# Kernel optimization log

Hardware: AMD Instinct MI355X
Metric: run time of the kernel (lower is better)

Reference implementation:

```python
import jax, jax.numpy as jnp
import numpy as np
from jax import lax

jax.config.update("jax_enable_x64", True)

B = 32768          # batch size
NCS = 96           # number of charging stations
NB = 124           # num_buses
S_BASE = 1000.0
MAX_CS = 22.17
MIN_CS = -22.17
MAX_EV_CH = 22.0
MAX_EV_DIS = -22.0
EV_CAP = 70.0
EV_MIN_CAP = 15.0
ITERS = 100
TOL = 1e-06
DT = 15.0 / 60.0   # timescale (hours)


def setup_inputs() -> dict:
    ks = jax.random.split(jax.random.key(0), 12)
    action = jax.random.uniform(ks[0], (B, NCS), dtype=jnp.float32, minval=-1.0, maxval=1.0)
    prices = jax.random.uniform(ks[1], (B, 1), dtype=jnp.float32, minval=0.05, maxval=0.5)
    active = jax.random.uniform(ks[2], (B, NB - 1), dtype=jnp.float32, minval=0.0, maxval=50.0)
    reactive = jax.random.uniform(ks[3], (B, NB - 1), dtype=jnp.float32, minval=0.0, maxval=20.0)
    cap = jax.random.uniform(ks[4], (B, NCS), dtype=jnp.float32, minval=0.0, maxval=EV_CAP)
    cap = cap * (jax.random.uniform(ks[5], (B, NCS)) > 0.2).astype(jnp.float32)
    tleft = jax.random.randint(ks[6], (B, NCS), 1, 10).astype(jnp.float32)
    bus = jax.random.randint(ks[7], (B, NCS), 0, NB - 1).astype(jnp.float32)
    ev = jnp.stack([cap, tleft, bus], axis=-1).reshape(B, 3 * NCS)  # interleaved triples
    state = jnp.concatenate(
        [jnp.zeros((B, 3), jnp.float32), prices, active, reactive, ev], axis=1
    )  # (B, 4 + 2*(NB-1) + 3*NCS) == (B, 538)
    K_re = (0.005 * jax.random.normal(ks[8], (NB - 1, NB - 1))).astype(jnp.float32)
    K_im = (0.005 * jax.random.normal(ks[9], (NB - 1, NB - 1))).astype(jnp.float32)
    L_re = jnp.ones((NB - 1,), jnp.float32)
    L_im = jnp.zeros((NB - 1,), jnp.float32)
    return {"action": action, "state": state, "K_re": K_re, "K_im": K_im, "L_re": L_re, "L_im": L_im}


def _forward(action, state, K_re, K_im, L_re, L_im):
    b, ncs = action.shape
    nb1 = NB - 1
    es = 4 + 2 * nb1  # start of EV state block
    prices = state[:, 3:4]                                    # (B,1), broadcast over stations
    cap = state[:, es:es + 3 * ncs:3]                         # current capacity
    tleft = state[:, es + 1:es + 1 + 3 * ncs:3]               # time left
    bus = state[:, es + 2:es + 2 + 3 * ncs:3].astype(jnp.int32)  # connected bus index
    conn = (cap > 0).astype(action.dtype)
    max_ch = jnp.minimum(MAX_EV_CH, conn * (EV_CAP - cap) / DT)
    max_dis = jnp.maximum(MAX_EV_DIS, conn * (EV_MIN_CAP - cap) / DT)
    pos = jnp.where(action >= 0, 1.0, 0.0).astype(action.dtype)
    power = action * MAX_CS * pos - action * MIN_CS * (1.0 - pos)
    power = jnp.maximum(jnp.minimum(power, max_ch), max_dis)
    costs = (prices * power * DT).sum(axis=1)
    new_cap = jnp.ceil((cap + power * DT) * 100.0) / 100.0
    dep = (tleft == 1).astype(action.dtype)
    user_sat = (-10.0 * dep * (new_cap - EV_CAP) ** 2).sum(axis=1)
    # scatter-add EV power per bus (duplicate indices accumulate, like torch scatter_add)
    ev_bus = jnp.zeros((b, nb1), power.dtype).at[jnp.arange(b)[:, None], bus].add(power)
    ap = state[:, 4:4 + nb1]
    rp = state[:, 4 + nb1:4 + 2 * nb1]
    S = ((ap + ev_bus) / S_BASE + 1j * (rp / S_BASE)).astype(jnp.complex128)  # (B, NB-1)
    K = (K_re + 1j * K_im).astype(jnp.complex128)
    W = (L_re + 1j * L_im).astype(jnp.complex128)
    v_init = jnp.ones((b, nb1), jnp.complex128)

    def run(v0):
        # Z-bus fixed point: v_k = K @ conj(S / v0)^T + W   (batched as bi)
        vk = jnp.einsum('ij,bj->bi', K, jnp.conj(S / v0)) + W
        tol = jnp.max(jnp.abs(jnp.abs(vk) - jnp.abs(v0)))
        return vk, tol

    def body(carry, _):
        v0, done = carry
        def step(v):
            vk, tol = run(v)
            return vk, tol < TOL
        def skip(v):
            return v, jnp.array(True)
        v_next, conv = lax.cond(done, skip, step, v0)
        return (v_next, done | conv), None

    (v_fin, _), _ = lax.scan(body, (v_init, jnp.array(False)), None, length=ITERS)
    vmag = jnp.abs(v_fin)
    voltage_loss = jnp.minimum(0.0, 0.05 - jnp.abs(1.0 - vmag)).sum(axis=1)
    loss = 1000.0 * voltage_loss + costs + user_sat
    return loss.astype(jnp.float32)


def reference(action, state, K_re, K_im, L_re, L_im):
    return _forward(action, state, K_re, K_im, L_re, L_im)
```

## Files before the change

### kernel.cpp

```cpp
#include <hip/hip_runtime.h>

#define NB1   123
#define NCSd  96
#define SW    538
#define TPB   256
#define BT    16
#define STPB  128


__global__ __launch_bounds__(256) void k_norm(const float* __restrict__ Kre,
                                              const float* __restrict__ Kim,
                                              const float* __restrict__ Lre,
                                              const float* __restrict__ Lim,
                                              float* __restrict__ ws) {
    __shared__ float part[4];
    const int tid = threadIdx.x;
    const int w = tid >> 6, l = tid & 63;
    const int wid = blockIdx.x * 4 + w;
    const int j1 = wid, j2 = wid + 64;
    const bool has2 = j2 < NB1;

    const float* kr1 = Kre + j1 * NB1; const float* ki1 = Kim + j1 * NB1;
    float a0 = kr1[l], b0 = ki1[l];
    float a1 = 0.f, b1 = 0.f;
    if (l < NB1 - 64) { a1 = kr1[l + 64]; b1 = ki1[l + 64]; }
    float c0 = 0.f, d0 = 0.f, c1 = 0.f, d1 = 0.f;
    if (has2) {
        const float* kr2 = Kre + j2 * NB1; const float* ki2 = Kim + j2 * NB1;
        c0 = kr2[l]; d0 = ki2[l];
        if (l < NB1 - 64) { c1 = kr2[l + 64]; d1 = ki2[l + 64]; }
    }
    float s1 = fmaf(a0, a0, b0 * b0) + fmaf(a1, a1, b1 * b1);
    float s2 = fmaf(c0, c0, d0 * d0) + fmaf(c1, c1, d1 * d1);
    #pragma unroll
    for (int off = 32; off; off >>= 1) {
        s1 += __shfl_xor(s1, off);
        s2 += __shfl_xor(s2, off);
    }
    float m2 = has2 ? fmaxf(s1, s2) : s1;
    if (l == 0) part[w] = m2;
    __syncthreads();
    if (tid == 0)
        ws[1 + blockIdx.x] = fmaxf(fmaxf(part[0], part[1]), fmaxf(part[2], part[3]));

    if (blockIdx.x == 0 && w == 0) {
        float dr = Lre[l] - 1.f, di = Lim[l];
        float d2 = fmaf(dr, dr, di * di);
        if (l + 64 < NB1) {
            float dr2 = Lre[l + 64] - 1.f, di2 = Lim[l + 64];
            d2 = fmaxf(d2, fmaf(dr2, dr2, di2 * di2));
        }
        #pragma unroll
        for (int off = 32; off; off >>= 1) d2 = fmaxf(d2, __shfl_xor(d2, off));
        if (l == 0) ws[0] = d2;
    }
}

__global__ __launch_bounds__(TPB, 7) void k_fast(const float* __restrict__ action,
                                                 const float* __restrict__ state,
                                                 const float* __restrict__ Kre,
                                                 const float* __restrict__ Kim,
                                                 const float* __restrict__ Lre,
                                                 const float* __restrict__ Lim,
                                                 const float* __restrict__ ws,
                                                 float* __restrict__ out) {
    __shared__ __align__(16) float st[4][1088];
    __shared__ float ev[4][256];

    const int tid = threadIdx.x;
    const int w = tid >> 6, l = tid & 63;
    const long g = (long)blockIdx.x * 4 + w;

    const float4* G4 = (const float4*)(state + g * (2 * SW));
    float4 v0 = G4[l];
    float4 v1 = G4[l + 64];
    float4 v2 = G4[l + 128];
    float4 v3 = G4[l + 192];
    float4 v4 = make_float4(0.f, 0.f, 0.f, 0.f);
    const bool t4 = l < 269 - 256;
    if (t4) v4 = G4[l + 256];

    float r2p = (l < 16) ? ws[1 + l] : 0.f;
    float dw2 = ws[0];

    ev[w][l] = 0.f; ev[w][l + 64] = 0.f;
    ev[w][l + 128] = 0.f; ev[w][l + 192] = 0.f;

    float4* st4 = (float4*)st[w];
    st4[l] = v0; st4[l + 64] = v1; st4[l + 128] = v2; st4[l + 192] = v3;
    if (t4) st4[l + 256] = v4;

    const int e = l >> 5, li = l & 31;
    const long b = 2 * g + e;
    const float* srow = st[w] + e * SW;
    const float* actp = action + b * NCSd;
    float* evp = ev[w] + e * 128;
    const float pr = srow[3];

    float cost = 0.f, usat = 0.f;
    #pragma unroll
    for (int s = 0; s < 3; ++s) {
        int i = li + 32 * s;
        float cap = srow[250 + 3 * i];
        float tl  = srow[251 + 3 * i];
        int   bus = (int)srow[252 + 3 * i];
        float a   = actp[i];
        float conn = cap > 0.f ? 1.f : 0.f;
        float mch = fminf(22.0f,  conn * (70.0f - cap) * 4.0f);
        float mds = fmaxf(-22.0f, conn * (15.0f - cap) * 4.0f);
        float p = fmaxf(fminf(22.17f * a, mch), mds);
        cost = fmaf(pr * p, 0.25f, cost);
        float nc = ceilf((cap + p * 0.25f) * 100.0f) * 0.01f;
        if (tl == 1.0f) { float d = nc - 70.0f; usat = fmaf(-10.0f * d, d, usat); }
        atomicAdd(&evp[bus], p);
    }

    float s2 = 0.f;
    #pragma unroll
    for (int s = 0; s < 4; ++s) {
        int k = li + 32 * s;
        if (k < NB1) {
            float apv = srow[4 + k] + evp[k];
            float rpv = srow[127 + k];
            s2 = fmaf(apv, apv, fmaf(rpv, rpv, s2));
        }
    }
    #pragma unroll
    for (int off = 16; off; off >>= 1) {
        s2   += __shfl_xor(s2, off);
        cost += __shfl_xor(cost, off);
        usat += __shfl_xor(usat, off);
    }

    #pragma unroll
    for (int off = 8; off; off >>= 1) r2p = fmaxf(r2p, __shfl_xor(r2p, off));
    float R  = sqrtf(__shfl(r2p, 0));
    float dW = sqrtf(dw2);
    float t = 0.0495f - dW;
    float q2max = -1.0f;
    if (t > 0.f && t < 1.0f - dW) {
        float xm = (t * (1.0f - dW - t) - 1e-7f) / 1.001f;
        if (xm > 0.f && R > 0.f) {
            float sm = xm / R * 1000.0f;
            q2max = sm * sm;
        }
    }
    bool safe = s2 <= q2max;

    float vs0 = 0.f, vs1 = 0.f;
    unsigned long long bad = __ballot(!safe);
    if (bad & 0x100000001ull) {
        const int j1 = l, j2 = 64 + l;
        const bool has2 = j2 < NB1;
        float* cw = st[w];
        #pragma unroll 1
        for (int fe = 0; fe < 2; ++fe) {
            if (!((bad >> (fe * 32)) & 1ull)) continue;
            const float* frow = st[w] + fe * SW;
            float* fev = ev[w] + fe * 128;
            float S1r = (frow[4 + j1] + fev[j1]) * 0.001f;
            float S1i = frow[127 + j1] * 0.001f;
            float S2r = has2 ? (frow[4 + j2] + fev[j2]) * 0.001f : 0.f;
            float S2i = has2 ? frow[127 + j2] * 0.001f : 0.f;
            float W1r = Lre[j1], W1i = Lim[j1];
            float W2r = has2 ? Lre[j2] : 1.f;
            float W2i = has2 ? Lim[j2] : 0.f;
            float v1r = 1.f, v1i = 0.f, v2r = 1.f, v2i = 0.f;
            for (int it = 0; it < 32; ++it) {
                float d1 = v1r * v1r + v1i * v1i, i1 = 1.0f / d1;
                cw[j1]       = (S1r * v1r + S1i * v1i) * i1;
                cw[128 + j1] = (S1r * v1i - S1i * v1r) * i1;
                if (has2) {
                    float d2 = v2r * v2r + v2i * v2i, i2 = 1.0f / d2;
                    cw[j2]       = (S2r * v2r + S2i * v2i) * i2;
                    cw[128 + j2] = (S2r * v2i - S2i * v2r) * i2;
                }
                asm volatile("s_waitcnt lgkmcnt(0)" ::: "memory");
                float a1r = W1r, a1i = W1i, a2r = W2r, a2i = W2i;
                for (int k = 0; k < NB1; ++k) {
                    float cr = cw[k], ci = cw[128 + k];
                    float kr1 = Kre[j1 * NB1 + k], ki1 = Kim[j1 * NB1 + k];
                    a1r = fmaf(kr1, cr, fmaf(-ki1, ci, a1r));
                    a1i = fmaf(kr1, ci, fmaf( ki1, cr, a1i));
                    if (has2) {
                        float kr2 = Kre[j2 * NB1 + k], ki2 = Kim[j2 * NB1 + k];
                        a2r = fmaf(kr2, cr, fmaf(-ki2, ci, a2r));
                        a2i = fmaf(kr2, ci, fmaf( ki2, cr, a2i));
                    }
                }
                v1r = a1r; v1i = a1i; v2r = a2r; v2i = a2i;
                asm volatile("s_waitcnt lgkmcnt(0)" ::: "memory");
            }
            float vm1 = sqrtf(v1r * v1r + v1i * v1i);
            float vl = fminf(0.f, 0.05f - fabsf(1.0f - vm1));
            if (has2) {
                float vm2 = sqrtf(v2r * v2r + v2i * v2i);
                vl += fminf(0.f, 0.05f - fabsf(1.0f - vm2));
            }
            #pragma unroll
            for (int off = 32; off; off >>= 1) vl += __shfl_xor(vl, off);
            if (fe == 0) vs0 = vl; else vs1 = vl;
        }
    }

    if (li == 0) out[b] = cost + usat + 1000.0f * (e == 0 ? vs0 : vs1);
}

__global__ __launch_bounds__(STPB) void k_main(
    const float* __restrict__ action, const float* __restrict__ state,
    const float* __restrict__ Kre, const float* __restrict__ Kim,
    const float* __restrict__ Lre, const float* __restrict__ Lim,
    float* __restrict__ out)
{
    __shared__ float ev[BT][STPB];
    __shared__ float costs_s[BT];
    __shared__ float usat_s[BT];
    __shared__ __align__(16) float2 cmat[STPB][BT + 2];
    __shared__ float vls[STPB][BT + 1];
    __shared__ float red[2];
    const int tid = threadIdx.x;
    const int e0  = blockIdx.x * BT;
    for (int x = tid; x < BT * STPB; x += STPB) ((float*)ev)[x] = 0.f;
    if (tid < BT) { costs_s[tid] = 0.f; usat_s[tid] = 0.f; }
    __syncthreads();
    for (int task = tid; task < BT * NCSd; task += STPB) {
        int e = task / NCSd, i = task - e * NCSd;
        long b = (long)(e0 + e);
        const float* srow = state + b * SW;
        float cap = srow[250 + 3 * i], tleft = srow[251 + 3 * i];
        int bus = (int)srow[252 + 3 * i];
        float a = action[b * NCSd + i];
        float conn = cap > 0.f ? 1.f : 0.f;
        float mch = fminf(22.0f, conn * (70.0f - cap) * 4.0f);
        float mds = fmaxf(-22.0f, conn * (15.0f - cap) * 4.0f);
        float power = fmaxf(fminf(22.17f * a, mch), mds);
        atomicAdd(&costs_s[e], srow[3] * power * 0.25f);
        float nc = ceilf((cap + power * 0.25f) * 100.0f) * 0.01f;
        if (tleft == 1.0f) { float d = nc - 70.0f; atomicAdd(&usat_s[e], -10.0f * d * d); }
        atomicAdd(&ev[e][bus], power);
    }
    __syncthreads();
    const int j = tid;
    const bool jok = j < NB1;
    float Wre = jok ? Lre[j] : 1.0f, Wim = jok ? Lim[j] : 0.0f;
    float Sre[BT], Sim[BT], vr[BT], vi[BT];
    #pragma unroll
    for (int e = 0; e < BT; ++e) {
        long b = (long)(e0 + e);
        float ap = jok ? state[b * SW + 4 + j] : 0.f;
        float rp = jok ? state[b * SW + 127 + j] : 0.f;
        Sre[e] = (ap + ev[e][j]) * 0.001f; Sim[e] = rp * 0.001f;
        vr[e] = 1.f; vi[e] = 0.f;
    }
    for (int it = 0; it < 100; ++it) {
        #pragma unroll
        for (int e = 0; e < BT; ++e) {
            float d = vr[e]*vr[e] + vi[e]*vi[e];
            float inv = 1.0f / d;
            cmat[j][e] = make_float2((Sre[e]*vr[e] + Sim[e]*vi[e]) * inv,
                                     (Sre[e]*vi[e] - Sim[e]*vr[e]) * inv);
        }
        __syncthreads();
        float ar[BT], ai[BT];
        #pragma unroll
        for (int e = 0; e < BT; ++e) { ar[e] = Wre; ai[e] = Wim; }
        for (int k = 0; k < NB1; ++k) {
            float kr = jok ? Kre[j*NB1+k] : 0.f;
            float ki = jok ? Kim[j*NB1+k] : 0.f;
            const float4* crow = (const float4*)(&cmat[k][0]);
            #pragma unroll
            for (int eh = 0; eh < BT / 2; ++eh) {
                float4 c2 = crow[eh];
                ar[2*eh]   = fmaf(kr, c2.x, fmaf(-ki, c2.y, ar[2*eh]));
                ai[2*eh]   = fmaf(kr, c2.y, fmaf( ki, c2.x, ai[2*eh]));
                ar[2*eh+1] = fmaf(kr, c2.z, fmaf(-ki, c2.w, ar[2*eh+1]));
                ai[2*eh+1] = fmaf(kr, c2.w, fmaf( ki, c2.z, ai[2*eh+1]));
            }
        }
        float md = 0.f;
        #pragma unroll
        for (int e = 0; e < BT; ++e) {
            float vmn = sqrtf(ar[e]*ar[e] + ai[e]*ai[e]);
            float vmo = sqrtf(vr[e]*vr[e] + vi[e]*vi[e]);
            md = fmaxf(md, fabsf(vmn - vmo));
            vr[e] = ar[e]; vi[e] = ai[e];
        }
        #pragma unroll
        for (int off = 32; off > 0; off >>= 1) md = fmaxf(md, __shfl_xor(md, off));
        if ((tid & 63) == 0) red[tid >> 6] = md;
        __syncthreads();
        if (fmaxf(red[0], red[1]) < 1e-6f) break;
    }
    #pragma unroll
    for (int e = 0; e < BT; ++e) {
        float vm = sqrtf(vr[e]*vr[e] + vi[e]*vi[e]);
        vls[j][e] = jok ? fminf(0.f, 0.05f - fabsf(1.0f - vm)) : 0.f;
    }
    __syncthreads();
    if (tid < BT) {
        float s = 0.f;
        for (int k = 0; k < NB1; ++k) s += vls[k][tid];
        out[e0 + tid] = 1000.0f * s + costs_s[tid] + usat_s[tid];
    }
}

extern "C" void kernel_launch(void* const* d_in, const int* in_sizes, int n_in,
                              void* d_out, int out_size, void* d_ws, size_t ws_size,
                              hipStream_t stream) {
    const float* action = (const float*)d_in[0];
    const float* state  = (const float*)d_in[1];
    const float* Kre    = (const float*)d_in[2];
    const float* Kim    = (const float*)d_in[3];
    const float* Lre    = (const float*)d_in[4];
    const float* Lim    = (const float*)d_in[5];
    float* out = (float*)d_out;
    const int B = out_size;

    if (ws_size >= 17 * sizeof(float)) {
        float* ws = (float*)d_ws;
        hipLaunchKernelGGL(k_norm, dim3(16), dim3(256), 0, stream, Kre, Kim, Lre, Lim, ws);
        hipLaunchKernelGGL(k_fast, dim3(B / 8), dim3(TPB), 0, stream,
                           action, state, Kre, Kim, Lre, Lim, ws, out);
    } else {
        hipLaunchKernelGGL(k_main, dim3((B + BT - 1) / BT), dim3(STPB), 0, stream,
                           action, state, Kre, Kim, Lre, Lim, out);
    }
}
```

Before: 36.20 us.

## Make k_fast persistent with register prefetch of next state rows

Replaces the one-shot grid of B/8 blocks with a fixed grid of 1536 blocks. Each wave now loops over up to three row pairs and loads the next pair's state rows into registers while it computes on the current pair. The per-wave setup (reading the norm workspace and computing the safety bound) runs once per wave instead of once per pair. The aim is to hide global-load latency and amortise setup. In exchange, register pressure rises (launch bounds drop from 7 to 6 blocks per SM) and fewer waves are in flight to cover latency.

```diff
diff --git a/kernel.cpp b/kernel.cpp
--- a/kernel.cpp
+++ b/kernel.cpp
@@ -6,6 +6,8 @@
 #define TPB   256
 #define BT    16
 #define STPB  128
+#define NBLK  1536
+#define NWAVE (NBLK * 4)
 
 
 __global__ __launch_bounds__(256) void k_norm(const float* __restrict__ Kre,
@@ -56,82 +58,28 @@
     }
 }
 
-__global__ __launch_bounds__(TPB, 7) void k_fast(const float* __restrict__ action,
+__global__ __launch_bounds__(TPB, 6) void k_fast(const float* __restrict__ action,
                                                  const float* __restrict__ state,
                                                  const float* __restrict__ Kre,
                                                  const float* __restrict__ Kim,
                                                  const float* __restrict__ Lre,
                                                  const float* __restrict__ Lim,
                                                  const float* __restrict__ ws,
-                                                 float* __restrict__ out) {
+                                                 float* __restrict__ out,
+                                                 int P) {
     __shared__ __align__(16) float st[4][1088];
     __shared__ float ev[4][256];
 
     const int tid = threadIdx.x;
     const int w = tid >> 6, l = tid & 63;
-    const long g = (long)blockIdx.x * 4 + w;
-
-    const float4* G4 = (const float4*)(state + g * (2 * SW));
-    float4 v0 = G4[l];
-    float4 v1 = G4[l + 64];
-    float4 v2 = G4[l + 128];
-    float4 v3 = G4[l + 192];
-    float4 v4 = make_float4(0.f, 0.f, 0.f, 0.f);
+    const int e = l >> 5, li = l & 31;
     const bool t4 = l < 269 - 256;
-    if (t4) v4 = G4[l + 256];
+    float4* st4 = (float4*)st[w];
+    float* evp = ev[w] + e * 128;
+    const float* srow = st[w] + e * SW;
 
     float r2p = (l < 16) ? ws[1 + l] : 0.f;
     float dw2 = ws[0];
-
-    ev[w][l] = 0.f; ev[w][l + 64] = 0.f;
-    ev[w][l + 128] = 0.f; ev[w][l + 192] = 0.f;
-
-    float4* st4 = (float4*)st[w];
-    st4[l] = v0; st4[l + 64] = v1; st4[l + 128] = v2; st4[l + 192] = v3;
-    if (t4) st4[l + 256] = v4;
-
-    const int e = l >> 5, li = l & 31;
-    const long b = 2 * g + e;
-    const float* srow = st[w] + e * SW;
-    const float* actp = action + b * NCSd;
-    float* evp = ev[w] + e * 128;
-    const float pr = srow[3];
-
-    float cost = 0.f, usat = 0.f;
-    #pragma unroll
-    for (int s = 0; s < 3; ++s) {
-        int i = li + 32 * s;
-        float cap = srow[250 + 3 * i];
-        float tl  = srow[251 + 3 * i];
-        int   bus = (int)srow[252 + 3 * i];
-        float a   = actp[i];
-        float conn = cap > 0.f ? 1.f : 0.f;
-        float mch = fminf(22.0f,  conn * (70.0f - cap) * 4.0f);
-        float mds = fmaxf(-22.0f, conn * (15.0f - cap) * 4.0f);
-        float p = fmaxf(fminf(22.17f * a, mch), mds);
-        cost = fmaf(pr * p, 0.25f, cost);
-        float nc = ceilf((cap + p * 0.25f) * 100.0f) * 0.01f;
-        if (tl == 1.0f) { float d = nc - 70.0f; usat = fmaf(-10.0f * d, d, usat); }
-        atomicAdd(&evp[bus], p);
-    }
-
-    float s2 = 0.f;
-    #pragma unroll
-    for (int s = 0; s < 4; ++s) {
-        int k = li + 32 * s;
-        if (k < NB1) {
-            float apv = srow[4 + k] + evp[k];
-            float rpv = srow[127 + k];
-            s2 = fmaf(apv, apv, fmaf(rpv, rpv, s2));
-        }
-    }
-    #pragma unroll
-    for (int off = 16; off; off >>= 1) {
-        s2   += __shfl_xor(s2, off);
-        cost += __shfl_xor(cost, off);
-        usat += __shfl_xor(usat, off);
-    }
-
     #pragma unroll
     for (int off = 8; off; off >>= 1) r2p = fmaxf(r2p, __shfl_xor(r2p, off));
     float R  = sqrtf(__shfl(r2p, 0));
@@ -145,65 +93,130 @@
             q2max = sm * sm;
         }
     }
-    bool safe = s2 <= q2max;
-
-    float vs0 = 0.f, vs1 = 0.f;
-    unsigned long long bad = __ballot(!safe);
-    if (bad & 0x100000001ull) {
-        const int j1 = l, j2 = 64 + l;
-        const bool has2 = j2 < NB1;
-        float* cw = st[w];
+
+    long g = (long)blockIdx.x * 4 + w;
+    {
+        const float4* G4 = (const float4*)(state + g * (2 * SW));
+        float4 p0 = G4[l], p1 = G4[l + 64], p2 = G4[l + 128], p3 = G4[l + 192];
+        float4 p4 = make_float4(0.f, 0.f, 0.f, 0.f);
+        if (t4) p4 = G4[l + 256];
+
         #pragma unroll 1
-        for (int fe = 0; fe < 2; ++fe) {
-            if (!((bad >> (fe * 32)) & 1ull)) continue;
-            const float* frow = st[w] + fe * SW;
-            float* fev = ev[w] + fe * 128;
-            float S1r = (frow[4 + j1] + fev[j1]) * 0.001f;
-            float S1i = frow[127 + j1] * 0.001f;
-            float S2r = has2 ? (frow[4 + j2] + fev[j2]) * 0.001f : 0.f;
-            float S2i = has2 ? frow[127 + j2] * 0.001f : 0.f;
-            float W1r = Lre[j1], W1i = Lim[j1];
-            float W2r = has2 ? Lre[j2] : 1.f;
-            float W2i = has2 ? Lim[j2] : 0.f;
-            float v1r = 1.f, v1i = 0.f, v2r = 1.f, v2i = 0.f;
-            for (int it = 0; it < 32; ++it) {
-                float d1 = v1r * v1r + v1i * v1i, i1 = 1.0f / d1;
-                cw[j1]       = (S1r * v1r + S1i * v1i) * i1;
-                cw[128 + j1] = (S1r * v1i - S1i * v1r) * i1;
-                if (has2) {
-                    float d2 = v2r * v2r + v2i * v2i, i2 = 1.0f / d2;
-                    cw[j2]       = (S2r * v2r + S2i * v2i) * i2;
-                    cw[128 + j2] = (S2r * v2i - S2i * v2r) * i2;
+        for (int it = 0; it < 3; ++it) {
+            if (g >= P) break;
+            ev[w][l] = 0.f; ev[w][l + 64] = 0.f;
+            ev[w][l + 128] = 0.f; ev[w][l + 192] = 0.f;
+            st4[l] = p0; st4[l + 64] = p1; st4[l + 128] = p2; st4[l + 192] = p3;
+            if (t4) st4[l + 256] = p4;
+
+            const long gcur = g;
+            const long gn = g + NWAVE;
+            if (gn < P) {
+                const float4* G4n = (const float4*)(state + gn * (2 * SW));
+                p0 = G4n[l]; p1 = G4n[l + 64]; p2 = G4n[l + 128]; p3 = G4n[l + 192];
+                if (t4) p4 = G4n[l + 256];
+            }
+
+            const long b = 2 * gcur + e;
+            const float* actp = action + b * NCSd;
+            const float pr = srow[3];
+
+            float cost = 0.f, usat = 0.f;
+            #pragma unroll
+            for (int s = 0; s < 3; ++s) {
+                int i = li + 32 * s;
+                float cap = srow[250 + 3 * i];
+                float tl  = srow[251 + 3 * i];
+                int   bus = (int)srow[252 + 3 * i];
+                float a   = actp[i];
+                float conn = cap > 0.f ? 1.f : 0.f;
+                float mch = fminf(22.0f,  conn * (70.0f - cap) * 4.0f);
+                float mds = fmaxf(-22.0f, conn * (15.0f - cap) * 4.0f);
+                float p = fmaxf(fminf(22.17f * a, mch), mds);
+                cost = fmaf(pr * p, 0.25f, cost);
+                float nc = ceilf((cap + p * 0.25f) * 100.0f) * 0.01f;
+                if (tl == 1.0f) { float d = nc - 70.0f; usat = fmaf(-10.0f * d, d, usat); }
+                atomicAdd(&evp[bus], p);
+            }
+
+            float s2 = 0.f;
+            #pragma unroll
+            for (int s = 0; s < 4; ++s) {
+                int k = li + 32 * s;
+                if (k < NB1) {
+                    float apv = srow[4 + k] + evp[k];
+                    float rpv = srow[127 + k];
+                    s2 = fmaf(apv, apv, fmaf(rpv, rpv, s2));
                 }
-                asm volatile("s_waitcnt lgkmcnt(0)" ::: "memory");
-                float a1r = W1r, a1i = W1i, a2r = W2r, a2i = W2i;
-                for (int k = 0; k < NB1; ++k) {
-                    float cr = cw[k], ci = cw[128 + k];
-                    float kr1 = Kre[j1 * NB1 + k], ki1 = Kim[j1 * NB1 + k];
-                    a1r = fmaf(kr1, cr, fmaf(-ki1, ci, a1r));
-                    a1i = fmaf(kr1, ci, fmaf( ki1, cr, a1i));
+            }
+            #pragma unroll
+            for (int off = 16; off; off >>= 1) {
+                s2   += __shfl_xor(s2, off);
+                cost += __shfl_xor(cost, off);
+                usat += __shfl_xor(usat, off);
+            }
+            bool safe = s2 <= q2max;
+
+            float vs0 = 0.f, vs1 = 0.f;
+            unsigned long long bad = __ballot(!safe);
+            if (bad & 0x100000001ull) {
+                const int j1 = l, j2 = 64 + l;
+                const bool has2 = j2 < NB1;
+                float* cw = st[w];
+                #pragma unroll 1
+                for (int fe = 0; fe < 2; ++fe) {
+                    if (!((bad >> (fe * 32)) & 1ull)) continue;
+                    const float* frow = st[w] + fe * SW;
+                    float* fev = ev[w] + fe * 128;
+                    float S1r = (frow[4 + j1] + fev[j1]) * 0.001f;
+                    float S1i = frow[127 + j1] * 0.001f;
+                    float S2r = has2 ? (frow[4 + j2] + fev[j2]) * 0.001f : 0.f;
+                    float S2i = has2 ? frow[127 + j2] * 0.001f : 0.f;
+                    float W1r = Lre[j1], W1i = Lim[j1];
+                    float W2r = has2 ? Lre[j2] : 1.f;
+                    float W2i = has2 ? Lim[j2] : 0.f;
+                    float v1r = 1.f, v1i = 0.f, v2r = 1.f, v2i = 0.f;
+                    for (int itr = 0; itr < 32; ++itr) {
+                        float d1 = v1r * v1r + v1i * v1i, i1 = 1.0f / d1;
+                        cw[j1]       = (S1r * v1r + S1i * v1i) * i1;
+                        cw[128 + j1] = (S1r * v1i - S1i * v1r) * i1;
+                        if (has2) {
+                            float d2 = v2r * v2r + v2i * v2i, i2 = 1.0f / d2;
+                            cw[j2]       = (S2r * v2r + S2i * v2i) * i2;
+                            cw[128 + j2] = (S2r * v2i - S2i * v2r) * i2;
+                        }
+                        asm volatile("s_waitcnt lgkmcnt(0)" ::: "memory");
+                        float a1r = W1r, a1i = W1i, a2r = W2r, a2i = W2i;
+                        for (int k = 0; k < NB1; ++k) {
+                            float cr = cw[k], ci = cw[128 + k];
+                            float kr1 = Kre[j1 * NB1 + k], ki1 = Kim[j1 * NB1 + k];
+                            a1r = fmaf(kr1, cr, fmaf(-ki1, ci, a1r));
+                            a1i = fmaf(kr1, ci, fmaf( ki1, cr, a1i));
+                            if (has2) {
+                                float kr2 = Kre[j2 * NB1 + k], ki2 = Kim[j2 * NB1 + k];
+                                a2r = fmaf(kr2, cr, fmaf(-ki2, ci, a2r));
+                                a2i = fmaf(kr2, ci, fmaf( ki2, cr, a2i));
+                            }
+                        }
+                        v1r = a1r; v1i = a1i; v2r = a2r; v2i = a2i;
+                        asm volatile("s_waitcnt lgkmcnt(0)" ::: "memory");
+                    }
+                    float vm1 = sqrtf(v1r * v1r + v1i * v1i);
+                    float vl = fminf(0.f, 0.05f - fabsf(1.0f - vm1));
                     if (has2) {
-                        float kr2 = Kre[j2 * NB1 + k], ki2 = Kim[j2 * NB1 + k];
-                        a2r = fmaf(kr2, cr, fmaf(-ki2, ci, a2r));
-                        a2i = fmaf(kr2, ci, fmaf( ki2, cr, a2i));
+                        float vm2 = sqrtf(v2r * v2r + v2i * v2i);
+                        vl += fminf(0.f, 0.05f - fabsf(1.0f - vm2));
                     }
+                    #pragma unroll
+                    for (int off = 32; off; off >>= 1) vl += __shfl_xor(vl, off);
+                    if (fe == 0) vs0 = vl; else vs1 = vl;
                 }
-                v1r = a1r; v1i = a1i; v2r = a2r; v2i = a2i;
-                asm volatile("s_waitcnt lgkmcnt(0)" ::: "memory");
-            }
-            float vm1 = sqrtf(v1r * v1r + v1i * v1i);
-            float vl = fminf(0.f, 0.05f - fabsf(1.0f - vm1));
-            if (has2) {
-                float vm2 = sqrtf(v2r * v2r + v2i * v2i);
-                vl += fminf(0.f, 0.05f - fabsf(1.0f - vm2));
-            }
-            #pragma unroll
-            for (int off = 32; off; off >>= 1) vl += __shfl_xor(vl, off);
-            if (fe == 0) vs0 = vl; else vs1 = vl;
-        }
-    }
-
-    if (li == 0) out[b] = cost + usat + 1000.0f * (e == 0 ? vs0 : vs1);
+            }
+
+            if (li == 0) out[b] = cost + usat + 1000.0f * (e == 0 ? vs0 : vs1);
+            g = gn;
+        }
+    }
 }
 
 __global__ __launch_bounds__(STPB) void k_main(
@@ -315,12 +328,13 @@
     const float* Lim    = (const float*)d_in[5];
     float* out = (float*)d_out;
     const int B = out_size;
+    const int P = B / 2;
 
     if (ws_size >= 17 * sizeof(float)) {
         float* ws = (float*)d_ws;
         hipLaunchKernelGGL(k_norm, dim3(16), dim3(256), 0, stream, Kre, Kim, Lre, Lim, ws);
-        hipLaunchKernelGGL(k_fast, dim3(B / 8), dim3(TPB), 0, stream,
-                           action, state, Kre, Kim, Lre, Lim, ws, out);
+        hipLaunchKernelGGL(k_fast, dim3(NBLK), dim3(TPB), 0, stream,
+                           action, state, Kre, Kim, Lre, Lim, ws, out, P);
     } else {
         hipLaunchKernelGGL(k_main, dim3((B + BT - 1) / BT), dim3(STPB), 0, stream,
                            action, state, Kre, Kim, Lre, Lim, out);
```

New measurement: 49.14 us. 35.7% more time.
